# Performance work log

Measured on AMD Instinct MI355X. Metric: run time of the kernel, lower is better.

The kernel has to match this reference:

```python
import jax, jax.numpy as jnp
import numpy as np

H = 16      # num_attention_heads
D = 128     # head_size
ROT = 32    # rotary_ndims
WIN = 256   # attention_window[layer_id]
G = 64      # max_global_tokens
BASE = 10000.0


def _rotate_half(x):
    x1, x2 = jnp.split(x, 2, axis=-1)
    return jnp.concatenate([-x2, x1], axis=-1)


def setup_inputs() -> dict:
    key = jax.random.key(0)
    ks = jax.random.split(key, 6)
    B, S, HD = 2, 2048, H * D
    hidden_states = jax.random.normal(ks[0], (B, S, HD), jnp.float32)
    attention_mask = jnp.zeros((B, 1, 1, S), jnp.float32)
    glob_idx = jnp.sort(jax.random.randint(ks[1], (B, G), 0, S), axis=-1)
    W_qkv = jax.random.normal(ks[2], (HD, 3 * HD), jnp.float32) * 0.02
    b_qkv = jnp.zeros((3 * HD,), jnp.float32)
    W_o = jax.random.normal(ks[3], (HD, HD), jnp.float32) * 0.02
    b_o = jnp.zeros((HD,), jnp.float32)
    return {"hidden_states": hidden_states, "attention_mask": attention_mask,
            "glob_idx": glob_idx, "W_qkv": W_qkv, "b_qkv": b_qkv,
            "W_o": W_o, "b_o": b_o}


def reference(hidden_states, attention_mask, glob_idx, W_qkv, b_qkv, W_o, b_o):
    B, S, HD = hidden_states.shape
    qkv = (hidden_states @ W_qkv + b_qkv).reshape(B, S, H, 3 * D)
    q = qkv[..., :D].transpose(0, 2, 1, 3)        # [B,H,S,D]
    k = qkv[..., D:2 * D].transpose(0, 2, 1, 3)
    v = qkv[..., 2 * D:].transpose(0, 2, 1, 3)

    # GPT-NeoX rotary on first ROT dims
    inv_freq = 1.0 / (BASE ** (jnp.arange(0, ROT, 2, dtype=jnp.float32) / ROT))
    freqs = jnp.einsum('s,f->sf', jnp.arange(S, dtype=jnp.float32), inv_freq)
    emb = jnp.concatenate([freqs, freqs], axis=-1)           # [S,ROT]
    cos = jnp.cos(emb)[None, None]
    sin = jnp.sin(emb)[None, None]
    q = jnp.concatenate([q[..., :ROT] * cos + _rotate_half(q[..., :ROT]) * sin,
                         q[..., ROT:]], axis=-1)
    k = jnp.concatenate([k[..., :ROT] * cos + _rotate_half(k[..., :ROT]) * sin,
                         k[..., ROT:]], axis=-1)

    # step_attn path: keys/values are head-averaged before attention (key.mean(1))
    k_mean = k.mean(axis=1)   # [B,S,D]
    v_mean = v.mean(axis=1)
    scale = 1.0 / jnp.sqrt(jnp.float32(D))
    minv = jnp.finfo(jnp.float32).min

    s0 = jnp.einsum('bhqd,bkd->bhqk', q[:, :, :WIN], k_mean[:, :WIN]) * scale
    causal = jnp.tril(jnp.ones((WIN, WIN), bool))
    s0 = jnp.where(causal[None, None], s0, minv) + attention_mask[..., :WIN]
    out0 = jnp.einsum('bhqk,bkd->bhqd', jax.nn.softmax(s0, axis=-1), v_mean[:, :WIN])

    Sq = S - WIN
    steps = jnp.arange(Sq)
    win_pos = steps[:, None] + 1 + jnp.arange(WIN)[None, :]
    k_win = k_mean[:, win_pos]
    v_win = v_mean[:, win_pos]
    mask_win = attention_mask[:, 0, 0, :][:, win_pos][:, None]
    qs = q[:, :, WIN:]                                        # [B,H,Sq,D]
    s_win = jnp.einsum('bhqd,bqwd->bhqw', qs, k_win) * scale + mask_win

    k_glob = jnp.take_along_axis(k_mean, glob_idx[..., None], axis=1)  # [B,G,D]
    v_glob = jnp.take_along_axis(v_mean, glob_idx[..., None], axis=1)
    # sorted indices: 'filter < i then truncate to G' == prefix-valid mask per slot
    valid = (glob_idx[:, None, :] < steps[None, :, None])[:, None]     # [B,1,Sq,G]
    s_glob = jnp.where(valid, jnp.einsum('bhqd,bgd->bhqg', qs, k_glob) * scale, minv)

    w = jax.nn.softmax(jnp.concatenate([s_glob, s_win], axis=-1), axis=-1)
    out_steps = (jnp.einsum('bhqg,bgd->bhqd', w[..., :G], v_glob)
                 + jnp.einsum('bhqw,bqwd->bhqd', w[..., G:], v_win))

    out = jnp.concatenate([out0, out_steps], axis=2)          # [B,H,S,D]
    out = out.transpose(0, 2, 1, 3).reshape(B, S, HD)
    return out @ W_o + b_o
```

## Files before the change

kernel.cpp:

```cpp
#include <hip/hip_runtime.h>
#include <math.h>

#define SCALE_ 0.08838834764831845f
#define MINV_  (-3.4028234663852886e38f)

typedef __bf16 bf16;
typedef bf16  bf16x4 __attribute__((ext_vector_type(4)));
typedef bf16  bf16x8 __attribute__((ext_vector_type(8)));
typedef float f32x4  __attribute__((ext_vector_type(4)));
typedef float f32x16 __attribute__((ext_vector_type(16)));
typedef float float4v __attribute__((ext_vector_type(4)));

#define LD8(p) (*(const bf16x8*)(p))

__device__ __forceinline__ f32x4 mfma16(bf16x8 a, bf16x8 b, f32x4 c) {
    return __builtin_amdgcn_mfma_f32_16x16x32_bf16(a, b, c, 0, 0, 0);
}
__device__ __forceinline__ f32x16 mfma32(bf16x8 a, bf16x8 b, f32x16 c) {
    return __builtin_amdgcn_mfma_f32_32x32x16_bf16(a, b, c, 0, 0, 0);
}

typedef const __attribute__((address_space(1))) void* gas_t;
typedef __attribute__((address_space(3))) void* sas_t;
__device__ __forceinline__ void gload_lds16(const void* g, void* l) {
    __builtin_amdgcn_global_load_lds((gas_t)g, (sas_t)l, 16, 0, 0);
}


__global__ __launch_bounds__(256) void cast_hidden_kernel(const float* __restrict__ X, bf16* __restrict__ Y)
{
    int i = (blockIdx.x * 256 + threadIdx.x) * 4;
    float4v v = *(const float4v*)(X + i);
    bf16x4 o; o.x = (bf16)v.x; o.y = (bf16)v.y; o.z = (bf16)v.z; o.w = (bf16)v.w;
    *(bf16x4*)(Y + i) = o;
}

__global__ __launch_bounds__(256) void transpose_cast2_kernel(const float* __restrict__ Wqkv, bf16* __restrict__ BT1,
                                                              const float* __restrict__ Wo, bf16* __restrict__ BT2)
{
    __shared__ float tile[32][33];
    int z = blockIdx.z;
    const float* W = z ? Wo : Wqkv;
    bf16* BT = z ? BT2 : BT1;
    int srcStride = z ? 2048 : 6144;
    int k0 = blockIdx.x * 32, n0 = blockIdx.y * 32;
    int c = threadIdx.x & 31, r = threadIdx.x >> 5;
    int n = n0 + c;
    int src = z ? n : ((n >> 7) * 384 + (n & 127));
    #pragma unroll
    for (int rr = 0; rr < 32; rr += 8)
        tile[r + rr][c] = W[(size_t)(k0 + r + rr) * srcStride + src];
    __syncthreads();
    #pragma unroll
    for (int rr = 0; rr < 32; rr += 8)
        BT[(size_t)(n0 + r + rr) * 2048 + k0 + c] = (bf16)tile[c][r + rr];
}

__global__ __launch_bounds__(256) void bt1_kv_kernel(const float* __restrict__ Wqkv, const float* __restrict__ bqkv,
                                                     bf16* __restrict__ BT1, float* __restrict__ bias1)
{
    if (blockIdx.x == 512) {
        for (int c = threadIdx.x; c < 2304; c += 256) {
            if (c < 2048) bias1[c] = bqkv[(c >> 7) * 384 + (c & 127)];
            else {
                int j = c - 2048; float s = 0.f;
                for (int h = 0; h < 16; h++) s += bqkv[h * 384 + 128 + j];
                bias1[c] = s * 0.0625f;
            }
        }
        return;
    }
    int k0 = blockIdx.x * 4;
    int j = threadIdx.x;
    float acc[4];
    #pragma unroll
    for (int k = 0; k < 4; k++) acc[k] = 0.f;
    for (int h = 0; h < 16; h++) {
        #pragma unroll
        for (int k = 0; k < 4; k++)
            acc[k] += Wqkv[(size_t)(k0 + k) * 6144 + h * 384 + 128 + j];
    }
    #pragma unroll
    for (int k = 0; k < 4; k++)
        BT1[(size_t)(2048 + j) * 2048 + k0 + k] = (bf16)(acc[k] * 0.0625f);
}


#define GEMM_PROLOGUE_AND_KLOOP                                                           \
    __shared__ __align__(16) bf16 As[128 * 64];                                           \
    __shared__ __align__(16) bf16 Bs[128 * 64];                                           \
    const int tid  = threadIdx.x;                                                         \
    const int wv   = tid >> 6, lane = tid & 63, l32 = lane & 31, half = lane >> 5;        \
    const int wrow = wv >> 1, wcol = wv & 1;                                              \
    const int m0 = blockIdx.y * 128, n0 = blockIdx.x * 128;                               \
    int rowS[4], colS[4];                                                                 \
    _Pragma("unroll")                                                                     \
    for (int j = 0; j < 4; j++) {                                                         \
        int flat = (wv * 4 + j) * 64 + lane;                                              \
        int row = flat >> 3, cp = flat & 7;                                               \
        rowS[j] = row;                                                                    \
        colS[j] = (cp ^ (row & 7)) * 8;                                                   \
    }                                                                                     \
    f32x16 acc[2][2];                                                                     \
    _Pragma("unroll")                                                                     \
    for (int i = 0; i < 2; i++)                                                           \
        _Pragma("unroll")                                                                 \
        for (int j = 0; j < 2; j++)                                                       \
            _Pragma("unroll")                                                             \
            for (int r = 0; r < 16; r++) acc[i][j][r] = 0.f;                              \
    for (int kk = 0; kk < K; kk += 64) {                                                  \
        __syncthreads();                                                                  \
        _Pragma("unroll")                                                                 \
        for (int j = 0; j < 4; j++) {                                                     \
            gload_lds16(A  + (size_t)(m0 + rowS[j]) * K + kk + colS[j], &As[(wv * 4 + j) * 512]); \
            gload_lds16(BT + (size_t)(n0 + rowS[j]) * K + kk + colS[j], &Bs[(wv * 4 + j) * 512]); \
        }                                                                                 \
        __syncthreads();                                                                  \
        bf16x8 af[2][4], bfr[2][4];                                                       \
        _Pragma("unroll")                                                                 \
        for (int mt = 0; mt < 2; mt++) {                                                  \
            int row = wrow * 64 + mt * 32 + l32;                                          \
            _Pragma("unroll")                                                             \
            for (int k16 = 0; k16 < 4; k16++) {                                           \
                int lc = k16 * 2 + half;                                                  \
                af[mt][k16] = LD8(&As[row * 64 + ((lc ^ (row & 7)) * 8)]);                \
            }                                                                             \
        }                                                                                 \
        _Pragma("unroll")                                                                 \
        for (int nt = 0; nt < 2; nt++) {                                                  \
            int row = wcol * 64 + nt * 32 + l32;                                          \
            _Pragma("unroll")                                                             \
            for (int k16 = 0; k16 < 4; k16++) {                                           \
                int lc = k16 * 2 + half;                                                  \
                bfr[nt][k16] = LD8(&Bs[row * 64 + ((lc ^ (row & 7)) * 8)]);               \
            }                                                                             \
        }                                                                                 \
        _Pragma("unroll")                                                                 \
        for (int k16 = 0; k16 < 4; k16++)                                                 \
            _Pragma("unroll")                                                             \
            for (int mt = 0; mt < 2; mt++)                                                \
                _Pragma("unroll")                                                         \
                for (int nt = 0; nt < 2; nt++)                                            \
                    acc[mt][nt] = mfma32(af[mt][k16], bfr[nt][k16], acc[mt][nt]);         \
    }

__global__ __launch_bounds__(256) void gemm_rot_kernel(const bf16* __restrict__ A, const bf16* __restrict__ BT,
                                                       const float* __restrict__ bias, bf16* __restrict__ C,
                                                       int M, int N, int K)
{
    GEMM_PROLOGUE_AND_KLOOP

    #pragma unroll
    for (int mt = 0; mt < 2; mt++) {
        #pragma unroll
        for (int nt = 0; nt < 2; nt++) {
            int n = n0 + wcol * 64 + nt * 32 + l32;
            float bn = bias[n];
            const bool rot = (wcol == 0) && (nt == 0) && (n0 <= 2048);
            float inv = rot ? __expf(-0.575646273248511f * (float)(l32 & 15)) : 0.f;
            #pragma unroll
            for (int r = 0; r < 16; r++) {
                int m = m0 + wrow * 64 + mt * 32 + (r & 3) + 8 * (r >> 2) + 4 * half;
                float v = acc[mt][nt][r] + bn;
                if (rot) {
                    float ang = (float)(m & 2047) * inv;
                    float cs, sn;
                    __sincosf(ang, &sn, &cs);
                    float pv = __shfl_xor(v, 16, 64);
                    v = (l32 < 16) ? (v * cs - pv * sn) : (v * cs + pv * sn);
                }
                C[(size_t)m * N + n] = (bf16)v;
            }
        }
    }
}

__global__ __launch_bounds__(256) void gemm_out_kernel(const bf16* __restrict__ A, const bf16* __restrict__ BT,
                                                       const float* __restrict__ bias, float* __restrict__ C,
                                                       int M, int N, int K)
{
    GEMM_PROLOGUE_AND_KLOOP

    #pragma unroll
    for (int mt = 0; mt < 2; mt++) {
        #pragma unroll
        for (int nt = 0; nt < 2; nt++) {
            int n = n0 + wcol * 64 + nt * 32 + l32;
            float bn = bias[n];
            #pragma unroll
            for (int r = 0; r < 16; r++) {
                int m = m0 + wrow * 64 + mt * 32 + (r & 3) + 8 * (r >> 2) + 4 * half;
                C[(size_t)m * N + n] = acc[mt][nt][r] + bn;
            }
        }
    }
}

__global__ __launch_bounds__(256) void build_vmT_kernel(const bf16* __restrict__ C1, bf16* __restrict__ vmT)
{
    __shared__ float tile[32][33];
    int b = blockIdx.z;
    int s0 = blockIdx.x * 32, d0 = blockIdx.y * 32;
    int c = threadIdx.x & 31, r = threadIdx.x >> 5;
    #pragma unroll
    for (int rr = 0; rr < 32; rr += 8)
        tile[r + rr][c] = (float)C1[(size_t)(b * 2048 + s0 + r + rr) * 2304 + 2176 + d0 + c];
    __syncthreads();
    #pragma unroll
    for (int rr = 0; rr < 32; rr += 8)
        vmT[(size_t)(b * 128 + d0 + r + rr) * 2048 + s0 + c] = (bf16)tile[c][r + rr];
}

__global__ __launch_bounds__(256) void pretile_kernel(const bf16* __restrict__ C1, const bf16* __restrict__ vmT,
                                                      const int* __restrict__ gidx,
                                                      bf16* __restrict__ KF, bf16* __restrict__ VF)
{
    int c = blockIdx.x, b = blockIdx.z;
    bool isGlob = (c == 32);
    int sid = threadIdx.x + blockIdx.y * 256;
    int lane = sid & 63, fi = (sid >> 6) & 15;
    int l16 = lane & 15, quad = lane >> 4;
    if (sid < 1024) {
        int t = fi >> 2, ks = fi & 3;
        int pos = isGlob ? gidx[b * 64 + t * 16 + l16] : (c * 64 + t * 16 + l16);
        const bf16* src = C1 + (size_t)(b * 2048 + pos) * 2304 + 2048 + ks * 32 + quad * 8;
        *(bf16x8*)&KF[((size_t)(b * 33 + c) * 16 + fi) * 512 + lane * 8] = LD8(src);
    } else {
        int dt = fi >> 1, ks2 = fi & 1;
        int d = dt * 16 + l16;
        if (isGlob) {
            bf16 tmp[8];
            #pragma unroll
            for (int j = 0; j < 8; j++) {
                int pos = gidx[b * 64 + ks2 * 32 + quad * 8 + j];
                tmp[j] = vmT[(size_t)(b * 128 + d) * 2048 + pos];
            }
            #pragma unroll
            for (int j = 0; j < 8; j++)
                VF[((size_t)(b * 33 + 32) * 16 + fi) * 512 + lane * 8 + j] = tmp[j];
        } else {
            const bf16* src = vmT + (size_t)(b * 128 + d) * 2048 + c * 64 + ks2 * 32 + quad * 8;
            *(bf16x8*)&VF[((size_t)(b * 33 + c) * 16 + fi) * 512 + lane * 8] = LD8(src);
        }
    }
}

#define PSTRIDE 88

__device__ __forceinline__ void attn0_body(int bx, int h, int b, bf16* Pw,
                                           const bf16* __restrict__ C1, const bf16* __restrict__ KF,
                                           const bf16* __restrict__ VF, const float* __restrict__ mask,
                                           bf16* __restrict__ attn)
{
    const int tid = threadIdx.x, wv = tid >> 6, lane = tid & 63, quad = lane >> 4, l16 = lane & 15;
    const int q0 = (bx * 4 + wv) * 16;

    bf16x8 af[4];
    const bf16* qbase = C1 + (size_t)(b * 2048 + q0 + l16) * 2304 + h * 128;
    #pragma unroll
    for (int ks = 0; ks < 4; ks++) af[ks] = LD8(qbase + ks * 32 + quad * 8);

    f32x4 m_run = (f32x4){MINV_, MINV_, MINV_, MINV_};
    f32x4 l_run = (f32x4){0.f, 0.f, 0.f, 0.f};
    f32x4 O[8];
    #pragma unroll
    for (int dt = 0; dt < 8; dt++) O[dt] = (f32x4){0.f, 0.f, 0.f, 0.f};

    for (int c = 0; c <= bx; c++) {
        const bf16* KFc = KF + ((size_t)(b * 33 + c) * 16) * 512;
        const bf16* VFc = VF + ((size_t)(b * 33 + c) * 16) * 512;

        f32x4 acc[4];
        #pragma unroll
        for (int t = 0; t < 4; t++) acc[t] = (f32x4){0.f, 0.f, 0.f, 0.f};
        __builtin_amdgcn_s_setprio(1);
        #pragma unroll
        for (int t = 0; t < 4; t++)
            #pragma unroll
            for (int ks = 0; ks < 4; ks++)
                acc[t] = mfma16(af[ks], LD8(KFc + (size_t)(t * 4 + ks) * 512 + lane * 8), acc[t]);
        __builtin_amdgcn_s_setprio(0);

        float sv[4][4];
        #pragma unroll
        for (int t = 0; t < 4; t++) {
            int key = c * 64 + t * 16 + l16;
            float addv = mask[b * 2048 + key];
            #pragma unroll
            for (int r = 0; r < 4; r++) {
                int q = q0 + quad * 4 + r;
                sv[t][r] = (key <= q) ? (acc[t][r] * SCALE_ + addv) : MINV_;
            }
        }

        f32x4 cm;
        #pragma unroll
        for (int r = 0; r < 4; r++) cm[r] = fmaxf(fmaxf(sv[0][r], sv[1][r]), fmaxf(sv[2][r], sv[3][r]));
        #pragma unroll
        for (int ms = 1; ms < 16; ms <<= 1)
            #pragma unroll
            for (int r = 0; r < 4; r++) cm[r] = fmaxf(cm[r], __shfl_xor(cm[r], ms, 64));

        f32x4 nm, alpha;
        #pragma unroll
        for (int r = 0; r < 4; r++) { nm[r] = fmaxf(m_run[r], cm[r]); alpha[r] = __expf(m_run[r] - nm[r]); }

        float pv[4][4];
        f32x4 cs = (f32x4){0.f, 0.f, 0.f, 0.f};
        #pragma unroll
        for (int t = 0; t < 4; t++)
            #pragma unroll
            for (int r = 0; r < 4; r++) {
                pv[t][r] = __expf(sv[t][r] - nm[r]);
                cs[r] += pv[t][r];
            }
        #pragma unroll
        for (int ms = 1; ms < 16; ms <<= 1)
            #pragma unroll
            for (int r = 0; r < 4; r++) cs[r] += __shfl_xor(cs[r], ms, 64);

        m_run = nm;
        #pragma unroll
        for (int r = 0; r < 4; r++) l_run[r] = l_run[r] * alpha[r] + cs[r];
        #pragma unroll
        for (int dt = 0; dt < 8; dt++)
            #pragma unroll
            for (int r = 0; r < 4; r++) O[dt][r] *= alpha[r];

        #pragma unroll
        for (int t = 0; t < 4; t++)
            #pragma unroll
            for (int r = 0; r < 4; r++)
                Pw[(quad * 4 + r) * PSTRIDE + t * 16 + l16] = (bf16)pv[t][r];
        bf16x8 pa0 = LD8(&Pw[l16 * PSTRIDE + quad * 8]);
        bf16x8 pa1 = LD8(&Pw[l16 * PSTRIDE + 32 + quad * 8]);

        __builtin_amdgcn_s_setprio(1);
        #pragma unroll
        for (int dt = 0; dt < 8; dt++) {
            O[dt] = mfma16(pa0, LD8(VFc + (size_t)(dt * 2 + 0) * 512 + lane * 8), O[dt]);
            O[dt] = mfma16(pa1, LD8(VFc + (size_t)(dt * 2 + 1) * 512 + lane * 8), O[dt]);
        }
        __builtin_amdgcn_s_setprio(0);
    }

    f32x4 invl;
    #pragma unroll
    for (int r = 0; r < 4; r++) invl[r] = 1.0f / l_run[r];
    #pragma unroll
    for (int dt = 0; dt < 8; dt++)
        #pragma unroll
        for (int r = 0; r < 4; r++) {
            int q = q0 + quad * 4 + r;
            attn[(size_t)(b * 2048 + q) * 2048 + h * 128 + dt * 16 + l16] = (bf16)(O[dt][r] * invl[r]);
        }
}

__device__ __forceinline__ void attn_steps_body(int sb, int b, bf16* Pw,
                                                const bf16* __restrict__ C1, const bf16* __restrict__ KF,
                                                const bf16* __restrict__ VF, const float* __restrict__ mask,
                                                const int* __restrict__ gidx, bf16* __restrict__ attn)
{
    const int tid = threadIdx.x, wv = tid >> 6, lane = tid & 63, quad = lane >> 4, l16 = lane & 15;
    const int step = sb * 4 + wv, p = 256 + step;

    bf16x8 af[4];
    const bf16* qrow = C1 + (size_t)(b * 2048 + p) * 2304;
    #pragma unroll
    for (int ks = 0; ks < 4; ks++) af[ks] = LD8(qrow + l16 * 128 + ks * 32 + quad * 8);

    int gix[4];
    #pragma unroll
    for (int t = 0; t < 4; t++) gix[t] = gidx[b * 64 + t * 16 + l16];

    f32x4 m_run = (f32x4){MINV_, MINV_, MINV_, MINV_};
    f32x4 l_run = (f32x4){0.f, 0.f, 0.f, 0.f};
    f32x4 O[8];
    #pragma unroll
    for (int dt = 0; dt < 8; dt++) O[dt] = (f32x4){0.f, 0.f, 0.f, 0.f};

    const int c0 = (step + 1) >> 6;

    for (int iter = 0; iter < 6; iter++) {
        int c;
        bool isGlob = (iter == 0);
        if (isGlob) c = 32;
        else { c = c0 + iter - 1; if (c > 31) break; }

        const bf16* KFc = KF + ((size_t)(b * 33 + c) * 16) * 512;
        const bf16* VFc = VF + ((size_t)(b * 33 + c) * 16) * 512;

        f32x4 acc[4];
        #pragma unroll
        for (int t = 0; t < 4; t++) acc[t] = (f32x4){0.f, 0.f, 0.f, 0.f};
        __builtin_amdgcn_s_setprio(1);
        #pragma unroll
        for (int t = 0; t < 4; t++)
            #pragma unroll
            for (int ks = 0; ks < 4; ks++)
                acc[t] = mfma16(af[ks], LD8(KFc + (size_t)(t * 4 + ks) * 512 + lane * 8), acc[t]);
        __builtin_amdgcn_s_setprio(0);

        float sv[4][4];
        bool vld[4];
        #pragma unroll
        for (int t = 0; t < 4; t++) {
            float addv = 0.f;
            if (isGlob) vld[t] = gix[t] < step;
            else {
                int pos = c * 64 + t * 16 + l16;
                vld[t] = (unsigned)(pos - step - 1) < 256u;
                addv = mask[b * 2048 + pos];
            }
            #pragma unroll
            for (int r = 0; r < 4; r++) sv[t][r] = vld[t] ? (acc[t][r] * SCALE_ + addv) : MINV_;
        }

        f32x4 cm;
        #pragma unroll
        for (int r = 0; r < 4; r++) cm[r] = fmaxf(fmaxf(sv[0][r], sv[1][r]), fmaxf(sv[2][r], sv[3][r]));
        #pragma unroll
        for (int ms = 1; ms < 16; ms <<= 1)
            #pragma unroll
            for (int r = 0; r < 4; r++) cm[r] = fmaxf(cm[r], __shfl_xor(cm[r], ms, 64));

        f32x4 nm, alpha;
        #pragma unroll
        for (int r = 0; r < 4; r++) { nm[r] = fmaxf(m_run[r], cm[r]); alpha[r] = __expf(m_run[r] - nm[r]); }

        float pv[4][4];
        f32x4 cs = (f32x4){0.f, 0.f, 0.f, 0.f};
        #pragma unroll
        for (int t = 0; t < 4; t++)
            #pragma unroll
            for (int r = 0; r < 4; r++) {
                pv[t][r] = vld[t] ? __expf(sv[t][r] - nm[r]) : 0.f;
                cs[r] += pv[t][r];
            }
        #pragma unroll
        for (int ms = 1; ms < 16; ms <<= 1)
            #pragma unroll
            for (int r = 0; r < 4; r++) cs[r] += __shfl_xor(cs[r], ms, 64);

        m_run = nm;
        #pragma unroll
        for (int r = 0; r < 4; r++) l_run[r] = l_run[r] * alpha[r] + cs[r];
        #pragma unroll
        for (int dt = 0; dt < 8; dt++)
            #pragma unroll
            for (int r = 0; r < 4; r++) O[dt][r] *= alpha[r];

        #pragma unroll
        for (int t = 0; t < 4; t++)
            #pragma unroll
            for (int r = 0; r < 4; r++)
                Pw[(quad * 4 + r) * PSTRIDE + t * 16 + l16] = (bf16)pv[t][r];
        bf16x8 pa0 = LD8(&Pw[l16 * PSTRIDE + quad * 8]);
        bf16x8 pa1 = LD8(&Pw[l16 * PSTRIDE + 32 + quad * 8]);

        __builtin_amdgcn_s_setprio(1);
        #pragma unroll
        for (int dt = 0; dt < 8; dt++) {
            O[dt] = mfma16(pa0, LD8(VFc + (size_t)(dt * 2 + 0) * 512 + lane * 8), O[dt]);
            O[dt] = mfma16(pa1, LD8(VFc + (size_t)(dt * 2 + 1) * 512 + lane * 8), O[dt]);
        }
        __builtin_amdgcn_s_setprio(0);
    }

    f32x4 invl;
    #pragma unroll
    for (int r = 0; r < 4; r++) invl[r] = 1.0f / l_run[r];
    #pragma unroll
    for (int dt = 0; dt < 8; dt++)
        #pragma unroll
        for (int r = 0; r < 4; r++) {
            int h = quad * 4 + r;
            attn[(size_t)(b * 2048 + p) * 2048 + h * 128 + dt * 16 + l16] = (bf16)(O[dt][r] * invl[r]);
        }
}

__global__ __launch_bounds__(256) void attn_all_kernel(const bf16* __restrict__ C1, const bf16* __restrict__ KF,
                                                       const bf16* __restrict__ VF, const float* __restrict__ mask,
                                                       const int* __restrict__ gidx, bf16* __restrict__ attn)
{
    __shared__ __align__(16) bf16 Ps[4 * 16 * PSTRIDE];
    const int wv = threadIdx.x >> 6;
    bf16* Pw = &Ps[wv * (16 * PSTRIDE)];
    if (blockIdx.x < 448) {
        attn_steps_body(blockIdx.x, blockIdx.y, Pw, C1, KF, VF, mask, gidx, attn);
    } else {
        int bi = blockIdx.x - 448;
        attn0_body(bi >> 4, bi & 15, blockIdx.y, Pw, C1, KF, VF, mask, attn);
    }
}

extern "C" void kernel_launch(void* const* d_in, const int* in_sizes, int n_in,
                              void* d_out, int out_size, void* d_ws, size_t ws_size,
                              hipStream_t stream)
{
    const float* hidden = (const float*)d_in[0];
    const float* amask  = (const float*)d_in[1];
    const int*   gidx   = (const int*)d_in[2];
    const float* Wqkv   = (const float*)d_in[3];
    const float* bqkv   = (const float*)d_in[4];
    const float* Wo     = (const float*)d_in[5];
    const float* bo     = (const float*)d_in[6];

    char* ws = (char*)d_ws;
    size_t off = 0;
    auto take = [&](size_t bytes) -> char* {
        char* p = ws + off;
        off = (off + bytes + 255) & ~(size_t)255;
        return p;
    };
    bf16*  A16   = (bf16*)take(4096ull * 2048 * 2);
    bf16*  BT1   = (bf16*)take(2304ull * 2048 * 2);
    bf16*  BT2   = (bf16*)take(2048ull * 2048 * 2);
    bf16*  C1    = (bf16*)take(4096ull * 2304 * 2);
    bf16*  vmT   = (bf16*)take(2ull * 128 * 2048 * 2);
    bf16*  KF    = (bf16*)take(2ull * 33 * 16 * 512 * 2);
    bf16*  VF    = (bf16*)take(2ull * 33 * 16 * 512 * 2);
    bf16*  attnb = (bf16*)take(4096ull * 2048 * 2);
    float* bias1 = (float*)take(2304 * 4);

    cast_hidden_kernel<<<8192, 256, 0, stream>>>(hidden, A16);
    transpose_cast2_kernel<<<dim3(64, 64, 2), 256, 0, stream>>>(Wqkv, BT1, Wo, BT2);
    bt1_kv_kernel<<<513, 256, 0, stream>>>(Wqkv, bqkv, BT1, bias1);

    gemm_rot_kernel<<<dim3(18, 32), 256, 0, stream>>>(A16, BT1, bias1, C1, 4096, 2304, 2048);

    build_vmT_kernel<<<dim3(64, 4, 2), 256, 0, stream>>>(C1, vmT);
    pretile_kernel<<<dim3(33, 8, 2), 256, 0, stream>>>(C1, vmT, gidx, KF, VF);

    attn_all_kernel<<<dim3(512, 2), 256, 0, stream>>>(C1, KF, VF, amask, gidx, attnb);

    gemm_out_kernel<<<dim3(16, 32), 256, 0, stream>>>(attnb, BT2, bo, (float*)d_out, 4096, 2048, 2048);

    (void)in_sizes; (void)n_in; (void)out_size; (void)ws_size;
}
```

Measured before the change: 316.2 us.

## Merge prep kernels, fold V transpose into pretile, drop setprio hints

Three weight/activation preparation kernels are merged into one launch that dispatches by block index. The separate global vmT transpose kernel is removed: pretile now stages the V rows into shared memory and builds the transposed fragments from there. This cuts two launches and one global round trip. The s_setprio hints around the MFMA loops in the attention kernels are also removed, which changes wave scheduling. The merged pretile kernel launches far fewer blocks, so it has less parallelism.

```diff
diff --git a/kernel.cpp b/kernel.cpp
--- a/kernel.cpp
+++ b/kernel.cpp
@@ -26,40 +26,42 @@
     __builtin_amdgcn_global_load_lds((gas_t)g, (sas_t)l, 16, 0, 0);
 }
 
-
-__global__ __launch_bounds__(256) void cast_hidden_kernel(const float* __restrict__ X, bf16* __restrict__ Y)
-{
-    int i = (blockIdx.x * 256 + threadIdx.x) * 4;
-    float4v v = *(const float4v*)(X + i);
-    bf16x4 o; o.x = (bf16)v.x; o.y = (bf16)v.y; o.z = (bf16)v.z; o.w = (bf16)v.w;
-    *(bf16x4*)(Y + i) = o;
-}
-
-__global__ __launch_bounds__(256) void transpose_cast2_kernel(const float* __restrict__ Wqkv, bf16* __restrict__ BT1,
-                                                              const float* __restrict__ Wo, bf16* __restrict__ BT2)
-{
-    __shared__ float tile[32][33];
-    int z = blockIdx.z;
-    const float* W = z ? Wo : Wqkv;
-    bf16* BT = z ? BT2 : BT1;
-    int srcStride = z ? 2048 : 6144;
-    int k0 = blockIdx.x * 32, n0 = blockIdx.y * 32;
-    int c = threadIdx.x & 31, r = threadIdx.x >> 5;
-    int n = n0 + c;
-    int src = z ? n : ((n >> 7) * 384 + (n & 127));
-    #pragma unroll
-    for (int rr = 0; rr < 32; rr += 8)
-        tile[r + rr][c] = W[(size_t)(k0 + r + rr) * srcStride + src];
-    __syncthreads();
-    #pragma unroll
-    for (int rr = 0; rr < 32; rr += 8)
-        BT[(size_t)(n0 + r + rr) * 2048 + k0 + c] = (bf16)tile[c][r + rr];
-}
-
-__global__ __launch_bounds__(256) void bt1_kv_kernel(const float* __restrict__ Wqkv, const float* __restrict__ bqkv,
-                                                     bf16* __restrict__ BT1, float* __restrict__ bias1)
-{
-    if (blockIdx.x == 512) {
+__global__ __launch_bounds__(256) void prep_kernel(const float* __restrict__ hidden, bf16* __restrict__ A16,
+                                                   const float* __restrict__ Wqkv, bf16* __restrict__ BT1,
+                                                   const float* __restrict__ Wo, bf16* __restrict__ BT2,
+                                                   const float* __restrict__ bqkv, float* __restrict__ bias1)
+{
+    int x = blockIdx.x;
+    if (x < 8192) {
+        int i = (x * 256 + threadIdx.x) * 4;
+        float4v v = *(const float4v*)(hidden + i);
+        bf16x4 o; o.x = (bf16)v.x; o.y = (bf16)v.y; o.z = (bf16)v.z; o.w = (bf16)v.w;
+        *(bf16x4*)(A16 + i) = o;
+        return;
+    }
+    if (x < 16384) {
+        __shared__ float tile[32][33];
+        int t = x - 8192;
+        int z = t >> 12;
+        int tt = t & 4095;
+        const float* W = z ? Wo : Wqkv;
+        bf16* BT = z ? BT2 : BT1;
+        int srcStride = z ? 2048 : 6144;
+        int k0 = (tt & 63) * 32, n0 = (tt >> 6) * 32;
+        int c = threadIdx.x & 31, r = threadIdx.x >> 5;
+        int n = n0 + c;
+        int src = z ? n : ((n >> 7) * 384 + (n & 127));
+        #pragma unroll
+        for (int rr = 0; rr < 32; rr += 8)
+            tile[r + rr][c] = W[(size_t)(k0 + r + rr) * srcStride + src];
+        __syncthreads();
+        #pragma unroll
+        for (int rr = 0; rr < 32; rr += 8)
+            BT[(size_t)(n0 + r + rr) * 2048 + k0 + c] = (bf16)tile[c][r + rr];
+        return;
+    }
+    int t = x - 16384;
+    if (t == 512) {
         for (int c = threadIdx.x; c < 2304; c += 256) {
             if (c < 2048) bias1[c] = bqkv[(c >> 7) * 384 + (c & 127)];
             else {
@@ -70,7 +72,7 @@
         }
         return;
     }
-    int k0 = blockIdx.x * 4;
+    int k0 = t * 4;
     int j = threadIdx.x;
     float acc[4];
     #pragma unroll
@@ -196,52 +198,47 @@
     }
 }
 
-__global__ __launch_bounds__(256) void build_vmT_kernel(const bf16* __restrict__ C1, bf16* __restrict__ vmT)
-{
-    __shared__ float tile[32][33];
-    int b = blockIdx.z;
-    int s0 = blockIdx.x * 32, d0 = blockIdx.y * 32;
-    int c = threadIdx.x & 31, r = threadIdx.x >> 5;
-    #pragma unroll
-    for (int rr = 0; rr < 32; rr += 8)
-        tile[r + rr][c] = (float)C1[(size_t)(b * 2048 + s0 + r + rr) * 2304 + 2176 + d0 + c];
+__global__ __launch_bounds__(256) void pretile_kernel(const bf16* __restrict__ C1, const int* __restrict__ gidx,
+                                                      bf16* __restrict__ KF, bf16* __restrict__ VF)
+{
+    __shared__ bf16 Vt[64][130];
+    const int c = blockIdx.x, b = blockIdx.y;
+    const bool isGlob = (c == 32);
+    const int tid = threadIdx.x;
+
+    {
+        int row = tid >> 2, cb = (tid & 3) * 32;
+        int pos = isGlob ? gidx[b * 64 + row] : (c * 64 + row);
+        const bf16* src = C1 + (size_t)(b * 2048 + pos) * 2304 + 2176 + cb;
+        #pragma unroll
+        for (int k = 0; k < 4; k++)
+            *(bf16x8*)&Vt[row][cb + k * 8] = LD8(src + k * 8);
+    }
     __syncthreads();
-    #pragma unroll
-    for (int rr = 0; rr < 32; rr += 8)
-        vmT[(size_t)(b * 128 + d0 + r + rr) * 2048 + s0 + c] = (bf16)tile[c][r + rr];
-}
-
-__global__ __launch_bounds__(256) void pretile_kernel(const bf16* __restrict__ C1, const bf16* __restrict__ vmT,
-                                                      const int* __restrict__ gidx,
-                                                      bf16* __restrict__ KF, bf16* __restrict__ VF)
-{
-    int c = blockIdx.x, b = blockIdx.z;
-    bool isGlob = (c == 32);
-    int sid = threadIdx.x + blockIdx.y * 256;
-    int lane = sid & 63, fi = (sid >> 6) & 15;
-    int l16 = lane & 15, quad = lane >> 4;
-    if (sid < 1024) {
+
+    #pragma unroll
+    for (int i = 0; i < 4; i++) {
+        int sid = tid + i * 256;
+        int lane = sid & 63, fi = sid >> 6;
+        int l16 = lane & 15, quad = lane >> 4;
         int t = fi >> 2, ks = fi & 3;
         int pos = isGlob ? gidx[b * 64 + t * 16 + l16] : (c * 64 + t * 16 + l16);
         const bf16* src = C1 + (size_t)(b * 2048 + pos) * 2304 + 2048 + ks * 32 + quad * 8;
         *(bf16x8*)&KF[((size_t)(b * 33 + c) * 16 + fi) * 512 + lane * 8] = LD8(src);
-    } else {
+    }
+
+    #pragma unroll
+    for (int i = 0; i < 4; i++) {
+        int sid = tid + i * 256;
+        int lane = sid & 63, fi = sid >> 6;
+        int l16 = lane & 15, quad = lane >> 4;
         int dt = fi >> 1, ks2 = fi & 1;
         int d = dt * 16 + l16;
-        if (isGlob) {
-            bf16 tmp[8];
-            #pragma unroll
-            for (int j = 0; j < 8; j++) {
-                int pos = gidx[b * 64 + ks2 * 32 + quad * 8 + j];
-                tmp[j] = vmT[(size_t)(b * 128 + d) * 2048 + pos];
-            }
-            #pragma unroll
-            for (int j = 0; j < 8; j++)
-                VF[((size_t)(b * 33 + 32) * 16 + fi) * 512 + lane * 8 + j] = tmp[j];
-        } else {
-            const bf16* src = vmT + (size_t)(b * 128 + d) * 2048 + c * 64 + ks2 * 32 + quad * 8;
-            *(bf16x8*)&VF[((size_t)(b * 33 + c) * 16 + fi) * 512 + lane * 8] = LD8(src);
-        }
+        bf16x8 v;
+        #pragma unroll
+        for (int j = 0; j < 8; j++)
+            v[j] = Vt[ks2 * 32 + quad * 8 + j][d];
+        *(bf16x8*)&VF[((size_t)(b * 33 + c) * 16 + fi) * 512 + lane * 8] = v;
     }
 }
 
@@ -273,13 +270,11 @@
         f32x4 acc[4];
         #pragma unroll
         for (int t = 0; t < 4; t++) acc[t] = (f32x4){0.f, 0.f, 0.f, 0.f};
-        __builtin_amdgcn_s_setprio(1);
         #pragma unroll
         for (int t = 0; t < 4; t++)
             #pragma unroll
             for (int ks = 0; ks < 4; ks++)
                 acc[t] = mfma16(af[ks], LD8(KFc + (size_t)(t * 4 + ks) * 512 + lane * 8), acc[t]);
-        __builtin_amdgcn_s_setprio(0);
 
         float sv[4][4];
         #pragma unroll
@@ -335,13 +330,11 @@
         bf16x8 pa0 = LD8(&Pw[l16 * PSTRIDE + quad * 8]);
         bf16x8 pa1 = LD8(&Pw[l16 * PSTRIDE + 32 + quad * 8]);
 
-        __builtin_amdgcn_s_setprio(1);
         #pragma unroll
         for (int dt = 0; dt < 8; dt++) {
             O[dt] = mfma16(pa0, LD8(VFc + (size_t)(dt * 2 + 0) * 512 + lane * 8), O[dt]);
             O[dt] = mfma16(pa1, LD8(VFc + (size_t)(dt * 2 + 1) * 512 + lane * 8), O[dt]);
         }
-        __builtin_amdgcn_s_setprio(0);
     }
 
     f32x4 invl;
@@ -393,13 +386,11 @@
         f32x4 acc[4];
         #pragma unroll
         for (int t = 0; t < 4; t++) acc[t] = (f32x4){0.f, 0.f, 0.f, 0.f};
-        __builtin_amdgcn_s_setprio(1);
         #pragma unroll
         for (int t = 0; t < 4; t++)
             #pragma unroll
             for (int ks = 0; ks < 4; ks++)
                 acc[t] = mfma16(af[ks], LD8(KFc + (size_t)(t * 4 + ks) * 512 + lane * 8), acc[t]);
-        __builtin_amdgcn_s_setprio(0);
 
         float sv[4][4];
         bool vld[4];
@@ -458,13 +449,11 @@
         bf16x8 pa0 = LD8(&Pw[l16 * PSTRIDE + quad * 8]);
         bf16x8 pa1 = LD8(&Pw[l16 * PSTRIDE + 32 + quad * 8]);
 
-        __builtin_amdgcn_s_setprio(1);
         #pragma unroll
         for (int dt = 0; dt < 8; dt++) {
             O[dt] = mfma16(pa0, LD8(VFc + (size_t)(dt * 2 + 0) * 512 + lane * 8), O[dt]);
             O[dt] = mfma16(pa1, LD8(VFc + (size_t)(dt * 2 + 1) * 512 + lane * 8), O[dt]);
         }
-        __builtin_amdgcn_s_setprio(0);
     }
 
     f32x4 invl;
@@ -517,20 +506,16 @@
     bf16*  BT1   = (bf16*)take(2304ull * 2048 * 2);
     bf16*  BT2   = (bf16*)take(2048ull * 2048 * 2);
     bf16*  C1    = (bf16*)take(4096ull * 2304 * 2);
-    bf16*  vmT   = (bf16*)take(2ull * 128 * 2048 * 2);
     bf16*  KF    = (bf16*)take(2ull * 33 * 16 * 512 * 2);
     bf16*  VF    = (bf16*)take(2ull * 33 * 16 * 512 * 2);
     bf16*  attnb = (bf16*)take(4096ull * 2048 * 2);
     float* bias1 = (float*)take(2304 * 4);
 
-    cast_hidden_kernel<<<8192, 256, 0, stream>>>(hidden, A16);
-    transpose_cast2_kernel<<<dim3(64, 64, 2), 256, 0, stream>>>(Wqkv, BT1, Wo, BT2);
-    bt1_kv_kernel<<<513, 256, 0, stream>>>(Wqkv, bqkv, BT1, bias1);
+    prep_kernel<<<16897, 256, 0, stream>>>(hidden, A16, Wqkv, BT1, Wo, BT2, bqkv, bias1);
 
     gemm_rot_kernel<<<dim3(18, 32), 256, 0, stream>>>(A16, BT1, bias1, C1, 4096, 2304, 2048);
 
-    build_vmT_kernel<<<dim3(64, 4, 2), 256, 0, stream>>>(C1, vmT);
-    pretile_kernel<<<dim3(33, 8, 2), 256, 0, stream>>>(C1, vmT, gidx, KF, VF);
+    pretile_kernel<<<dim3(33, 2), 256, 0, stream>>>(C1, gidx, KF, VF);
 
     attn_all_kernel<<<dim3(512, 2), 256, 0, stream>>>(C1, KF, VF, amask, gidx, attnb);
 
```

After: 303.2 us. -4.1%, faster.
